# Kernel tuning notes

Measured on AMD Instinct MI355X. Metric: run time of the kernel, lower is better.

Reference implementation:

```python
import jax, jax.numpy as jnp
import numpy as np

EPS = 1e-8

def _center(G):
    # Double-centering: H @ G @ H with H = I - 11^T/n, expressed as mean subtraction.
    # Identical math to the torch H-matmul version, O(n^2) instead of O(n^3).
    row = jnp.mean(G, axis=-1, keepdims=True)
    col = jnp.mean(G, axis=-2, keepdims=True)
    tot = jnp.mean(G, axis=(-2, -1), keepdims=True)
    return G - row - col + tot


def setup_inputs() -> dict:
    key = jax.random.key(0)
    k1, k2 = jax.random.split(key)
    B, L, H, M = 32, 128, 512, 512
    x = jax.random.normal(k1, (B, L, H), dtype=jnp.float32)
    # nn.Embedding.from_pretrained(torch.normal(-0.01, 0.2, (M, L*H)))
    centroid_w = jax.random.normal(k2, (M, L * H), dtype=jnp.float32) * 0.2 - 0.01
    return {"x": x, "centroid_w": centroid_w}


def reference(x, centroid_w):
    B, L, H = x.shape
    M = centroid_w.shape[0]
    cent = centroid_w.reshape(M, L, H)

    # Centered linear Grams
    Cx = _center(jnp.einsum('blh,bkh->blk', x, x))        # (B, L, L)
    Cy = _center(jnp.einsum('mlh,mkh->mlk', cent, cent))  # (M, L, L)

    # linear HSIC: sum over LxL of elementwise product -> (B, M)
    hsic = jnp.einsum('bij,mij->bm', Cx, Cy)
    vx = jnp.sqrt(jnp.sum(Cx * Cx, axis=(1, 2)))  # (B,)  sqrt(HSIC(x,x))
    vy = jnp.sqrt(jnp.sum(Cy * Cy, axis=(1, 2)))  # (M,)  sqrt(HSIC(y,y))
    cka_loss_matrix = -jnp.log(jnp.abs(hsic / (vx[:, None] * vy[None, :])) + EPS)

    idx = jnp.argmax(cka_loss_matrix, axis=-1)  # (B,)
    sel = cent[idx]                              # (B, L, H) gathered centroids

    # Second CKA pass against selected centroids; torch broadcasting makes (B, B)
    Cs = _center(jnp.einsum('blh,bkh->blk', sel, sel))  # (B, L, L)
    hsic2 = jnp.einsum('bij,cij->bc', Cx, Cs)           # (B, B)
    vs = jnp.sqrt(jnp.sum(Cs * Cs, axis=(1, 2)))        # (B,)
    cka_loss = -jnp.log(jnp.mean(jnp.abs(hsic2 / (vx[:, None] * vs[None, :]))) + EPS)

    return cka_loss, cka_loss_matrix, idx
```

## Files before the change

kernel.cpp:

```cpp
#include <hip/hip_runtime.h>
#include <math.h>

#define BB 32
#define LL 128
#define HH 512
#define MM 512
#define NM 544
#define EPSF 1e-8f
#define CPLEN 10240
#define NCH 40

typedef __attribute__((ext_vector_type(8))) short short8b;
typedef __attribute__((ext_vector_type(4))) float f32x4;
typedef __attribute__((ext_vector_type(16))) float f32x16;

#define NWS_CP    0
#define NWS_PART  5570560
#define NWS_NSQ   6225920
#define NWS_HSIC  6226464
#define NWS_IDS   6242848

__device__ __forceinline__ unsigned pack2(unsigned lo, unsigned hi) {
    return (lo >> 16) | (hi & 0xffff0000u);
}

__device__ __forceinline__ void split3(const float4 lo, const float4 hi,
                                       uint4& p0, uint4& p1, uint4& p2) {
    float c[8] = {lo.x, lo.y, lo.z, lo.w, hi.x, hi.y, hi.z, hi.w};
    unsigned h[8], m[8], l[8];
#pragma unroll
    for (int i = 0; i < 8; ++i) {
        h[i] = __float_as_uint(c[i]) & 0xffff0000u;
        const float r1 = c[i] - __uint_as_float(h[i]);
        m[i] = __float_as_uint(r1) & 0xffff0000u;
        l[i] = __float_as_uint(r1 - __uint_as_float(m[i]));
    }
    p0 = make_uint4(pack2(h[0],h[1]), pack2(h[2],h[3]), pack2(h[4],h[5]), pack2(h[6],h[7]));
    p1 = make_uint4(pack2(m[0],m[1]), pack2(m[2],m[3]), pack2(m[4],m[5]), pack2(m[6],m[7]));
    p2 = make_uint4(pack2(l[0],l[1]), pack2(l[2],l[3]), pack2(l[4],l[5]), pack2(l[6],l[7]));
}

__device__ __forceinline__ void mfma6(f32x16& d, const short8b a[3], const short8b b[3]) {
    d = __builtin_amdgcn_mfma_f32_32x32x16_bf16(a[0], b[0], d, 0, 0, 0);
    d = __builtin_amdgcn_mfma_f32_32x32x16_bf16(a[0], b[1], d, 0, 0, 0);
    d = __builtin_amdgcn_mfma_f32_32x32x16_bf16(a[1], b[0], d, 0, 0, 0);
    d = __builtin_amdgcn_mfma_f32_32x32x16_bf16(a[1], b[1], d, 0, 0, 0);
    d = __builtin_amdgcn_mfma_f32_32x32x16_bf16(a[0], b[2], d, 0, 0, 0);
    d = __builtin_amdgcn_mfma_f32_32x32x16_bf16(a[2], b[0], d, 0, 0, 0);
}

__device__ __forceinline__ int flatAB(int a, int b) {
    return ((a >> 3) * 2 + ((a >> 2) & 1)) * 128 + b * 4 + (a & 3);
}

__device__ __forceinline__ int Tix(int i, int j) {
    return i * (7 - i) / 2 + j;
}

__global__ __launch_bounds__(256, 2)
void gram_nb(const float* __restrict__ x,
             const float* __restrict__ cent,
             float* __restrict__ Cp,
             float* __restrict__ normsq)
{
    __shared__ union {
        uint4 stage[4][3][2][128];
        float buf[12288];
    } sm;
    __shared__ float rmv[128];
    __shared__ float red[256];
    __shared__ float gmsh;

    const int tid  = threadIdx.x;
    const int lane = tid & 63;
    const int wid  = tid >> 6;
    const int n    = blockIdx.x;
    const float* Amat = (n < BB) ? (x + (size_t)n * LL * HH)
                                 : (cent + (size_t)(n - BB) * LL * HH);

    const int o   = lane & 1;
    const int r2  = lane >> 1;
    const int kw  = wid * 128;

    f32x16 acc[10];
#pragma unroll
    for (int g = 0; g < 10; ++g)
#pragma unroll
        for (int q = 0; q < 16; ++q) acc[g][q] = 0.f;

    uint4* SW = &sm.stage[wid][0][0][0];

    float4 v0[4], v1[4];
#pragma unroll
    for (int p = 0; p < 4; ++p) {
        const float* rp = Amat + (size_t)(32 * p + r2) * HH + kw + o * 8;
        v0[p] = *(const float4*)rp;
        v1[p] = *(const float4*)(rp + 4);
    }

    for (int t = 0; t < 8; ++t) {
#pragma unroll
        for (int p = 0; p < 4; ++p) {
            uint4 q0, q1, q2;
            split3(v0[p], v1[p], q0, q1, q2);
            const int r = 32 * p + r2;
            SW[(0 * 2 + o) * 128 + r] = q0;
            SW[(1 * 2 + o) * 128 + r] = q1;
            SW[(2 * 2 + o) * 128 + r] = q2;
        }
        const int kn = kw + ((t < 7) ? (t + 1) * 16 : 112);
#pragma unroll
        for (int p = 0; p < 4; ++p) {
            const float* rp = Amat + (size_t)(32 * p + r2) * HH + kn + o * 8;
            v0[p] = *(const float4*)rp;
            v1[p] = *(const float4*)(rp + 4);
        }
        const int fo = lane >> 5, frr = lane & 31;
        short8b fr[4][3];
#pragma unroll
        for (int s = 0; s < 4; ++s)
#pragma unroll
            for (int pl = 0; pl < 3; ++pl) {
                uint4 u = SW[(pl * 2 + fo) * 128 + s * 32 + frr];
                fr[s][pl] = *(const short8b*)&u;
            }
        mfma6(acc[0], fr[0], fr[0]);
        mfma6(acc[1], fr[0], fr[1]);
        mfma6(acc[4], fr[1], fr[1]);
        mfma6(acc[2], fr[0], fr[2]);
        mfma6(acc[5], fr[1], fr[2]);
        mfma6(acc[7], fr[2], fr[2]);
        mfma6(acc[3], fr[0], fr[3]);
        mfma6(acc[6], fr[1], fr[3]);
        mfma6(acc[8], fr[2], fr[3]);
        mfma6(acc[9], fr[3], fr[3]);
    }

    __syncthreads();

    const int hi  = lane >> 5, col = lane & 31;
#pragma unroll
    for (int w = 0; w < 4; ++w) {
        if (wid == w) {
#pragma unroll
            for (int g = 0; g < 10; ++g)
#pragma unroll
                for (int c = 0; c < 4; ++c) {
                    const int idx = g * 1024 + (c * 2 + hi) * 128 + col * 4;
                    f32x4 a4;
                    a4[0] = acc[g][c * 4 + 0];
                    a4[1] = acc[g][c * 4 + 1];
                    a4[2] = acc[g][c * 4 + 2];
                    a4[3] = acc[g][c * 4 + 3];
                    if (w > 0) {
                        const f32x4 old = *(const f32x4*)&sm.buf[idx];
                        a4[0] += old[0]; a4[1] += old[1];
                        a4[2] += old[2]; a4[3] += old[3];
                    }
                    *(f32x4*)&sm.buf[idx] = a4;
                }
        }
        __syncthreads();
    }

    float s = 0.f;
    if (tid < 128) {
        const int i = tid >> 5, ri = tid & 31;
#pragma unroll
        for (int j = 0; j < 4; ++j) {
            if (j >= i) {
                const int g = Tix(i, j);
#pragma unroll
                for (int b = 0; b < 32; ++b)
                    s += sm.buf[g * 1024 + flatAB(ri, b)];
            } else {
                const int g = Tix(j, i);
#pragma unroll
                for (int a = 0; a < 32; ++a)
                    s += sm.buf[g * 1024 + flatAB(a, ri)];
            }
        }
        rmv[tid] = s * (1.f / 128.f);
    }
    red[tid] = (tid < 128) ? s : 0.f;
    __syncthreads();
    for (int s2 = 128; s2 > 0; s2 >>= 1) {
        if (tid < s2) red[tid] += red[tid + s2];
        __syncthreads();
    }
    if (tid == 0) gmsh = red[0] * (1.f / 16384.f);
    __syncthreads();
    const float gm = gmsh;

    const int b  = tid & 31;
    const int c2 = tid >> 5;
    const int ar = (c2 >> 1) * 8 + (c2 & 1) * 4;
    float nsq = 0.f;
    float* dstn = Cp + (size_t)n * CPLEN;
    static const int TI[10] = {0,0,0,0,1,1,1,2,2,3};
    static const int TJ[10] = {0,1,2,3,1,2,3,2,3,3};
#pragma unroll
    for (int g = 0; g < 10; ++g) {
        const int i = TI[g], j = TJ[g];
        const float sc = (i == j) ? 1.f : 1.41421356237309505f;
        const f32x4 vv = *(const f32x4*)&sm.buf[g * 1024 + tid * 4];
        const float4 rr = *(const float4*)&rmv[i * 32 + ar];
        const float riq[4] = {rr.x, rr.y, rr.z, rr.w};
        const float cj = rmv[j * 32 + b];
        f32x4 ov;
#pragma unroll
        for (int q = 0; q < 4; ++q) {
            const float val = (vv[q] + gm - riq[q] - cj) * sc;
            nsq = fmaf(val, val, nsq);
            ov[q] = val;
        }
        *(f32x4*)(dstn + g * 1024 + tid * 4) = ov;
    }
    __syncthreads();
    red[tid] = nsq;
    __syncthreads();
    for (int s2 = 128; s2 > 0; s2 >>= 1) {
        if (tid < s2) red[tid] += red[tid + s2];
        __syncthreads();
    }
    if (tid == 0) normsq[n] = red[0];
}

__global__ __launch_bounds__(256, 2)
void hsic_partial(const float* __restrict__ Cp, float* __restrict__ part)
{
    __shared__ float cx[32][260];
    __shared__ float red2[256][16];

    const int tid = threadIdx.x;
    const int bx  = blockIdx.x;
    const int mt  = bx / NCH;
    const int kc  = bx % NCH;
    const int k0  = kc * 256;

#pragma unroll
    for (int i = 0; i < 8; ++i) {
        const int idx = i * 1024 + tid * 4;
        const int b = idx >> 8, k = idx & 255;
        *(float4*)&cx[b][k] = *(const float4*)&Cp[(size_t)b * CPLEN + k0 + k];
    }
    __syncthreads();

    const int kq = tid >> 6;
    const int bg = (tid >> 3) & 7;
    const int mg = tid & 7;
    const float* cyBase = Cp + (size_t)(BB + mt * 32 + mg * 4) * CPLEN + k0 + kq * 64;

    float a[4][4];
#pragma unroll
    for (int bi = 0; bi < 4; ++bi)
#pragma unroll
        for (int mi = 0; mi < 4; ++mi) a[bi][mi] = 0.f;

    for (int kk = 0; kk < 16; ++kk) {
        float4 cy[4];
#pragma unroll
        for (int mi = 0; mi < 4; ++mi)
            cy[mi] = *(const float4*)(cyBase + (size_t)mi * CPLEN + kk * 4);
        float4 cxv[4];
#pragma unroll
        for (int bi = 0; bi < 4; ++bi)
            cxv[bi] = *(const float4*)&cx[bg + bi * 8][kq * 64 + kk * 4];
#pragma unroll
        for (int bi = 0; bi < 4; ++bi)
#pragma unroll
            for (int mi = 0; mi < 4; ++mi) {
                a[bi][mi] = fmaf(cxv[bi].x, cy[mi].x, a[bi][mi]);
                a[bi][mi] = fmaf(cxv[bi].y, cy[mi].y, a[bi][mi]);
                a[bi][mi] = fmaf(cxv[bi].z, cy[mi].z, a[bi][mi]);
                a[bi][mi] = fmaf(cxv[bi].w, cy[mi].w, a[bi][mi]);
            }
    }

#pragma unroll
    for (int e = 0; e < 16; ++e) red2[tid][e] = a[e >> 2][e & 3];
    __syncthreads();
    if (tid < 64) {
#pragma unroll
        for (int e = 0; e < 16; ++e) {
            const float s = red2[tid][e] + red2[tid + 64][e] +
                            red2[tid + 128][e] + red2[tid + 192][e];
            const int bi = e >> 2, mi = e & 3;
            const int b = ((tid >> 3) & 7) + bi * 8;
            const int m = mt * 32 + (tid & 7) * 4 + mi;
            part[((size_t)kc * 32 + b) * 512 + m] = s;
        }
    }
}

__global__ __launch_bounds__(256)
void combine_loss(const float* __restrict__ part,
                  const float* __restrict__ normsq,
                  float* __restrict__ hsic,
                  int* __restrict__ ids,
                  float* __restrict__ out)
{
    __shared__ float rv[256];
    __shared__ int   ri[256];
    const int b = blockIdx.x;
    const int tid = threadIdx.x;
    const float vx = sqrtf(normsq[b]);

    float best = -INFINITY; int bm = 0;
    for (int m = tid; m < MM; m += 256) {
        float s = 0.f;
        for (int kc = 0; kc < NCH; ++kc)
            s += part[((size_t)kc * 32 + b) * 512 + m];
        hsic[b * MM + m] = s;
        const float vy = sqrtf(normsq[BB + m]);
        const float loss = -logf(fabsf(s) / (vx * vy) + EPSF);
        out[1 + b * MM + m] = loss;
        if (loss > best) { best = loss; bm = m; }
    }
    rv[tid] = best; ri[tid] = bm;
    __syncthreads();
    for (int s2 = 128; s2 > 0; s2 >>= 1) {
        if (tid < s2) {
            if (rv[tid + s2] > rv[tid] ||
                (rv[tid + s2] == rv[tid] && ri[tid + s2] < ri[tid])) {
                rv[tid] = rv[tid + s2]; ri[tid] = ri[tid + s2];
            }
        }
        __syncthreads();
    }
    if (tid == 0) { ids[b] = ri[0]; out[1 + BB * MM + b] = (float)ri[0]; }
}

__global__ __launch_bounds__(1024)
void scalar_loss(const float* __restrict__ hsic,
                 const float* __restrict__ normsq,
                 const int* __restrict__ ids,
                 float* __restrict__ out)
{
    __shared__ float red[1024];
    const int tid = threadIdx.x;
    const int b = tid >> 5, c = tid & 31;
    const int m = ids[c];
    red[tid] = fabsf(hsic[b * MM + m]) /
               (sqrtf(normsq[b]) * sqrtf(normsq[BB + m]));
    __syncthreads();
    for (int s = 512; s > 0; s >>= 1) {
        if (tid < s) red[tid] += red[tid + s];
        __syncthreads();
    }
    if (tid == 0) out[0] = -logf(red[0] * (1.f / 1024.f) + EPSF);
}

extern "C" void kernel_launch(void* const* d_in, const int* in_sizes, int n_in,
                              void* d_out, int out_size, void* d_ws, size_t ws_size,
                              hipStream_t stream) {
    const float* x    = (const float*)d_in[0];
    const float* cent = (const float*)d_in[1];
    float* out = (float*)d_out;
    float* ws  = (float*)d_ws;

    float* Cp     = ws + NWS_CP;
    float* part   = ws + NWS_PART;
    float* normsq = ws + NWS_NSQ;
    float* hsic   = ws + NWS_HSIC;
    int*   ids    = (int*)(ws + NWS_IDS);

    gram_nb<<<NM, 256, 0, stream>>>(x, cent, Cp, normsq);
    hsic_partial<<<16 * NCH, 256, 0, stream>>>(Cp, part);
    combine_loss<<<BB, 256, 0, stream>>>(part, normsq, hsic, ids, out);
    scalar_loss<<<1, 1024, 0, stream>>>(hsic, normsq, ids, out);
}
```

Baseline: 98.05 us.

## Compute each Gram matrix in a single wave without LDS staging

Replaces the 4-wave Gram kernel, which split K across waves and reduced the partial Grams through shared memory, with a one-wave-per-matrix kernel. That wave loads fp32 rows straight into registers in MFMA fragment layout, double-buffers two K-steps, and does row and column means with cross-lane shuffles. The goal is to drop the LDS staging, the cross-wave reduction and the block barriers. The cost is that each matrix's whole K loop now runs serially on one wave. With 544 single-wave blocks the GPU runs far fewer waves, so memory latency and MFMA throughput per SIMD may be harder to hide.

```diff
diff --git a/kernel.cpp b/kernel.cpp
--- a/kernel.cpp
+++ b/kernel.cpp
@@ -20,6 +20,9 @@
 #define NWS_HSIC  6226464
 #define NWS_IDS   6242848
 
+__device__ __constant__ int TI_[10] = {0,0,0,0,1,1,1,2,2,3};
+__device__ __constant__ int TJ_[10] = {0,1,2,3,1,2,3,2,3,3};
+
 __device__ __forceinline__ unsigned pack2(unsigned lo, unsigned hi) {
     return (lo >> 16) | (hi & 0xffff0000u);
 }
@@ -40,47 +43,62 @@
     p2 = make_uint4(pack2(l[0],l[1]), pack2(l[2],l[3]), pack2(l[4],l[5]), pack2(l[6],l[7]));
 }
 
-__device__ __forceinline__ void mfma6(f32x16& d, const short8b a[3], const short8b b[3]) {
-    d = __builtin_amdgcn_mfma_f32_32x32x16_bf16(a[0], b[0], d, 0, 0, 0);
-    d = __builtin_amdgcn_mfma_f32_32x32x16_bf16(a[0], b[1], d, 0, 0, 0);
-    d = __builtin_amdgcn_mfma_f32_32x32x16_bf16(a[1], b[0], d, 0, 0, 0);
-    d = __builtin_amdgcn_mfma_f32_32x32x16_bf16(a[1], b[1], d, 0, 0, 0);
-    d = __builtin_amdgcn_mfma_f32_32x32x16_bf16(a[0], b[2], d, 0, 0, 0);
-    d = __builtin_amdgcn_mfma_f32_32x32x16_bf16(a[2], b[0], d, 0, 0, 0);
-}
-
-__device__ __forceinline__ int flatAB(int a, int b) {
-    return ((a >> 3) * 2 + ((a >> 2) & 1)) * 128 + b * 4 + (a & 3);
-}
-
-__device__ __forceinline__ int Tix(int i, int j) {
-    return i * (7 - i) / 2 + j;
-}
-
-__global__ __launch_bounds__(256, 2)
-void gram_nb(const float* __restrict__ x,
-             const float* __restrict__ cent,
-             float* __restrict__ Cp,
-             float* __restrict__ normsq)
+__device__ __forceinline__ float redxor5(float v) {
+    v += __shfl_xor(v, 1, 64);
+    v += __shfl_xor(v, 2, 64);
+    v += __shfl_xor(v, 4, 64);
+    v += __shfl_xor(v, 8, 64);
+    v += __shfl_xor(v, 16, 64);
+    return v;
+}
+
+#define LOADV(dst, t) do {                                                  \
+    _Pragma("unroll")                                                       \
+    for (int p_ = 0; p_ < 4; ++p_) {                                        \
+        const float* rp_ = Abase[p_] + (t) * 16;                            \
+        dst[2*p_]   = *(const float4*)rp_;                                  \
+        dst[2*p_+1] = *(const float4*)(rp_ + 4);                            \
+    } } while (0)
+
+#define SPLIT4(src, fr) do {                                                \
+    _Pragma("unroll")                                                       \
+    for (int p_ = 0; p_ < 4; ++p_) {                                        \
+        uint4 u0_, u1_, u2_;                                                \
+        split3(src[2*p_], src[2*p_+1], u0_, u1_, u2_);                      \
+        fr[p_][0] = *(short8b*)&u0_;                                        \
+        fr[p_][1] = *(short8b*)&u1_;                                        \
+        fr[p_][2] = *(short8b*)&u2_;                                        \
+    } } while (0)
+
+#define MFMA60(fr) do {                                                     \
+    const int PA_[6] = {0,0,1,1,0,2};                                       \
+    const int PB_[6] = {0,1,0,1,2,0};                                       \
+    _Pragma("unroll")                                                       \
+    for (int ps_ = 0; ps_ < 6; ++ps_) {                                     \
+        _Pragma("unroll")                                                   \
+        for (int g_ = 0; g_ < 10; ++g_)                                     \
+            acc[g_] = __builtin_amdgcn_mfma_f32_32x32x16_bf16(              \
+                fr[TI_[g_]][PA_[ps_]], fr[TJ_[g_]][PB_[ps_]], acc[g_], 0, 0, 0); \
+    } } while (0)
+
+__global__ __launch_bounds__(64, 1)
+void gram_wave(const float* __restrict__ x,
+               const float* __restrict__ cent,
+               float* __restrict__ Cp,
+               float* __restrict__ normsq)
 {
-    __shared__ union {
-        uint4 stage[4][3][2][128];
-        float buf[12288];
-    } sm;
-    __shared__ float rmv[128];
-    __shared__ float red[256];
-    __shared__ float gmsh;
-
-    const int tid  = threadIdx.x;
-    const int lane = tid & 63;
-    const int wid  = tid >> 6;
+    __shared__ __align__(16) float rowacc[128];
+
+    const int lane = threadIdx.x;
+    const int r32  = lane & 31;
+    const int oct  = lane >> 5;
     const int n    = blockIdx.x;
     const float* Amat = (n < BB) ? (x + (size_t)n * LL * HH)
                                  : (cent + (size_t)(n - BB) * LL * HH);
-
-    const int o   = lane & 1;
-    const int r2  = lane >> 1;
-    const int kw  = wid * 128;
+    const float* Abase[4];
+#pragma unroll
+    for (int p = 0; p < 4; ++p)
+        Abase[p] = Amat + (size_t)(32 * p + r32) * HH + oct * 8;
 
     f32x16 acc[10];
 #pragma unroll
@@ -88,142 +106,110 @@
 #pragma unroll
         for (int q = 0; q < 16; ++q) acc[g][q] = 0.f;
 
-    uint4* SW = &sm.stage[wid][0][0][0];
-
-    float4 v0[4], v1[4];
-#pragma unroll
-    for (int p = 0; p < 4; ++p) {
-        const float* rp = Amat + (size_t)(32 * p + r2) * HH + kw + o * 8;
-        v0[p] = *(const float4*)rp;
-        v1[p] = *(const float4*)(rp + 4);
-    }
-
-    for (int t = 0; t < 8; ++t) {
-#pragma unroll
-        for (int p = 0; p < 4; ++p) {
-            uint4 q0, q1, q2;
-            split3(v0[p], v1[p], q0, q1, q2);
-            const int r = 32 * p + r2;
-            SW[(0 * 2 + o) * 128 + r] = q0;
-            SW[(1 * 2 + o) * 128 + r] = q1;
-            SW[(2 * 2 + o) * 128 + r] = q2;
-        }
-        const int kn = kw + ((t < 7) ? (t + 1) * 16 : 112);
-#pragma unroll
-        for (int p = 0; p < 4; ++p) {
-            const float* rp = Amat + (size_t)(32 * p + r2) * HH + kn + o * 8;
-            v0[p] = *(const float4*)rp;
-            v1[p] = *(const float4*)(rp + 4);
-        }
-        const int fo = lane >> 5, frr = lane & 31;
-        short8b fr[4][3];
-#pragma unroll
-        for (int s = 0; s < 4; ++s)
-#pragma unroll
-            for (int pl = 0; pl < 3; ++pl) {
-                uint4 u = SW[(pl * 2 + fo) * 128 + s * 32 + frr];
-                fr[s][pl] = *(const short8b*)&u;
-            }
-        mfma6(acc[0], fr[0], fr[0]);
-        mfma6(acc[1], fr[0], fr[1]);
-        mfma6(acc[4], fr[1], fr[1]);
-        mfma6(acc[2], fr[0], fr[2]);
-        mfma6(acc[5], fr[1], fr[2]);
-        mfma6(acc[7], fr[2], fr[2]);
-        mfma6(acc[3], fr[0], fr[3]);
-        mfma6(acc[6], fr[1], fr[3]);
-        mfma6(acc[8], fr[2], fr[3]);
-        mfma6(acc[9], fr[3], fr[3]);
-    }
-
-    __syncthreads();
-
-    const int hi  = lane >> 5, col = lane & 31;
-#pragma unroll
-    for (int w = 0; w < 4; ++w) {
-        if (wid == w) {
+    float4 sA[8], sB[8];
+    short8b frA[4][3], frB[4][3];
+
+    LOADV(sA, 0);
+    LOADV(sB, 1);
+#pragma unroll 1
+    for (int tt = 0; tt < 16; ++tt) {
+        SPLIT4(sA, frA);
+        if (tt < 15) { LOADV(sA, 2 * tt + 2); }
+        MFMA60(frA);
+        SPLIT4(sB, frB);
+        if (tt < 15) { LOADV(sB, 2 * tt + 3); }
+        MFMA60(frB);
+    }
+
+#pragma unroll
+    for (int i = 0; i < 4; ++i) {
+        float rp[16];
+#pragma unroll
+        for (int q = 0; q < 16; ++q) {
+            float s = 0.f;
 #pragma unroll
             for (int g = 0; g < 10; ++g)
-#pragma unroll
-                for (int c = 0; c < 4; ++c) {
-                    const int idx = g * 1024 + (c * 2 + hi) * 128 + col * 4;
-                    f32x4 a4;
-                    a4[0] = acc[g][c * 4 + 0];
-                    a4[1] = acc[g][c * 4 + 1];
-                    a4[2] = acc[g][c * 4 + 2];
-                    a4[3] = acc[g][c * 4 + 3];
-                    if (w > 0) {
-                        const f32x4 old = *(const f32x4*)&sm.buf[idx];
-                        a4[0] += old[0]; a4[1] += old[1];
-                        a4[2] += old[2]; a4[3] += old[3];
-                    }
-                    *(f32x4*)&sm.buf[idx] = a4;
-                }
-        }
-        __syncthreads();
-    }
-
-    float s = 0.f;
-    if (tid < 128) {
-        const int i = tid >> 5, ri = tid & 31;
-#pragma unroll
-        for (int j = 0; j < 4; ++j) {
-            if (j >= i) {
-                const int g = Tix(i, j);
-#pragma unroll
-                for (int b = 0; b < 32; ++b)
-                    s += sm.buf[g * 1024 + flatAB(ri, b)];
-            } else {
-                const int g = Tix(j, i);
-#pragma unroll
-                for (int a = 0; a < 32; ++a)
-                    s += sm.buf[g * 1024 + flatAB(a, ri)];
-            }
-        }
-        rmv[tid] = s * (1.f / 128.f);
-    }
-    red[tid] = (tid < 128) ? s : 0.f;
-    __syncthreads();
-    for (int s2 = 128; s2 > 0; s2 >>= 1) {
-        if (tid < s2) red[tid] += red[tid + s2];
-        __syncthreads();
-    }
-    if (tid == 0) gmsh = red[0] * (1.f / 16384.f);
-    __syncthreads();
-    const float gm = gmsh;
-
-    const int b  = tid & 31;
-    const int c2 = tid >> 5;
-    const int ar = (c2 >> 1) * 8 + (c2 & 1) * 4;
+                if (TI_[g] == i) s += acc[g][q];
+            rp[q] = redxor5(s);
+        }
+        if (r32 == 0) {
+#pragma unroll
+            for (int q = 0; q < 16; ++q)
+                rowacc[i * 32 + (q & 3) + 8 * (q >> 2) + 4 * oct] = rp[q];
+        }
+    }
+    {
+        float cs1 = 0.f, cs2 = 0.f, cs3 = 0.f;
+#pragma unroll
+        for (int g = 0; g < 10; ++g) {
+            if (TI_[g] == TJ_[g]) continue;
+            float cp = 0.f;
+#pragma unroll
+            for (int q = 0; q < 16; ++q) cp += acc[g][q];
+            if (TJ_[g] == 1) cs1 += cp;
+            else if (TJ_[g] == 2) cs2 += cp;
+            else cs3 += cp;
+        }
+        cs1 += __shfl_xor(cs1, 32, 64);
+        cs2 += __shfl_xor(cs2, 32, 64);
+        cs3 += __shfl_xor(cs3, 32, 64);
+        if (oct == 0) {
+            rowacc[1 * 32 + r32] += cs1;
+            rowacc[2 * 32 + r32] += cs2;
+            rowacc[3 * 32 + r32] += cs3;
+        }
+    }
+
+    float tot = rowacc[lane] + rowacc[lane + 64];
+    tot += __shfl_xor(tot, 1, 64);
+    tot += __shfl_xor(tot, 2, 64);
+    tot += __shfl_xor(tot, 4, 64);
+    tot += __shfl_xor(tot, 8, 64);
+    tot += __shfl_xor(tot, 16, 64);
+    tot += __shfl_xor(tot, 32, 64);
+    const float gm = tot * (1.f / 16384.f);
+
+    f32x4 rim[4][4];
+#pragma unroll
+    for (int i = 0; i < 4; ++i)
+#pragma unroll
+        for (int c = 0; c < 4; ++c) {
+            const f32x4 rv = *(const f32x4*)&rowacc[i * 32 + 8 * c + 4 * oct];
+            rim[i][c][0] = gm - rv[0] * (1.f / 128.f);
+            rim[i][c][1] = gm - rv[1] * (1.f / 128.f);
+            rim[i][c][2] = gm - rv[2] * (1.f / 128.f);
+            rim[i][c][3] = gm - rv[3] * (1.f / 128.f);
+        }
+    float cjs[4];
+#pragma unroll
+    for (int j = 0; j < 4; ++j) cjs[j] = rowacc[j * 32 + r32] * (1.f / 128.f);
+
     float nsq = 0.f;
     float* dstn = Cp + (size_t)n * CPLEN;
-    static const int TI[10] = {0,0,0,0,1,1,1,2,2,3};
-    static const int TJ[10] = {0,1,2,3,1,2,3,2,3,3};
 #pragma unroll
     for (int g = 0; g < 10; ++g) {
-        const int i = TI[g], j = TJ[g];
+        const int i = TI_[g], j = TJ_[g];
         const float sc = (i == j) ? 1.f : 1.41421356237309505f;
-        const f32x4 vv = *(const f32x4*)&sm.buf[g * 1024 + tid * 4];
-        const float4 rr = *(const float4*)&rmv[i * 32 + ar];
-        const float riq[4] = {rr.x, rr.y, rr.z, rr.w};
-        const float cj = rmv[j * 32 + b];
-        f32x4 ov;
-#pragma unroll
-        for (int q = 0; q < 4; ++q) {
-            const float val = (vv[q] + gm - riq[q] - cj) * sc;
-            nsq = fmaf(val, val, nsq);
-            ov[q] = val;
-        }
-        *(f32x4*)(dstn + g * 1024 + tid * 4) = ov;
-    }
-    __syncthreads();
-    red[tid] = nsq;
-    __syncthreads();
-    for (int s2 = 128; s2 > 0; s2 >>= 1) {
-        if (tid < s2) red[tid] += red[tid + s2];
-        __syncthreads();
-    }
-    if (tid == 0) normsq[n] = red[0];
+        const float cj = cjs[j];
+#pragma unroll
+        for (int c = 0; c < 4; ++c) {
+            f32x4 o;
+#pragma unroll
+            for (int q = 0; q < 4; ++q) {
+                const float val = (acc[g][c * 4 + q] + rim[i][c][q] - cj) * sc;
+                nsq = fmaf(val, val, nsq);
+                o[q] = val;
+            }
+            *(f32x4*)(dstn + g * 1024 + (c * 2 + oct) * 128 + r32 * 4) = o;
+        }
+    }
+    nsq += __shfl_xor(nsq, 1, 64);
+    nsq += __shfl_xor(nsq, 2, 64);
+    nsq += __shfl_xor(nsq, 4, 64);
+    nsq += __shfl_xor(nsq, 8, 64);
+    nsq += __shfl_xor(nsq, 16, 64);
+    nsq += __shfl_xor(nsq, 32, 64);
+    if (lane == 0) normsq[n] = nsq;
 }
 
 __global__ __launch_bounds__(256, 2)
@@ -365,7 +351,7 @@
     float* hsic   = ws + NWS_HSIC;
     int*   ids    = (int*)(ws + NWS_IDS);
 
-    gram_nb<<<NM, 256, 0, stream>>>(x, cent, Cp, normsq);
+    gram_wave<<<NM, 64, 0, stream>>>(x, cent, Cp, normsq);
     hsic_partial<<<16 * NCH, 256, 0, stream>>>(Cp, part);
     combine_loss<<<BB, 256, 0, stream>>>(part, normsq, hsic, ids, out);
     scalar_loss<<<1, 1024, 0, stream>>>(hsic, normsq, ids, out);
```

After: 315.7 us. +222.0%, slower.

## Restructure gram kernel to 8 waves with tile-split MFMA and double-buffered staging

Applied to the files above, without the earlier changes.

The Gram kernel moves from 4 waves (each computing all 10 triangular tiles over its own K slice) to 8 waves in two K-halves. Within a half, the 4 waves share one double-buffered LDS stage and split the 10 tiles among themselves, 2-3 each. This cuts per-wave accumulator registers so more waves fit per CU, and reduces the cross-wave reduction to two passes. In exchange it adds a __syncthreads every K step and unequal work per wave.

```diff
diff --git a/kernel.cpp b/kernel.cpp
--- a/kernel.cpp
+++ b/kernel.cpp
@@ -49,142 +49,157 @@
     d = __builtin_amdgcn_mfma_f32_32x32x16_bf16(a[2], b[0], d, 0, 0, 0);
 }
 
+__device__ __forceinline__ void ldstrip(const uint4* P, int strip, int lane, short8b f[3]) {
+    const int s = lane >> 5;
+    const int r = strip * 32 + (lane & 31);
+#pragma unroll
+    for (int p = 0; p < 3; ++p) {
+        uint4 u = P[(p * 2 + s) * 128 + r];
+        f[p] = *(const short8b*)&u;
+    }
+}
+
 __device__ __forceinline__ int flatAB(int a, int b) {
     return ((a >> 3) * 2 + ((a >> 2) & 1)) * 128 + b * 4 + (a & 3);
 }
-
 __device__ __forceinline__ int Tix(int i, int j) {
     return i * (7 - i) / 2 + j;
 }
 
-__global__ __launch_bounds__(256, 2)
-void gram_nb(const float* __restrict__ x,
-             const float* __restrict__ cent,
-             float* __restrict__ Cp,
-             float* __restrict__ normsq)
+__device__ __forceinline__ void put_tile(float* buf, int slot, const f32x16& a,
+                                         int lane, bool add) {
+    const int hi = lane >> 5, col = lane & 31;
+#pragma unroll
+    for (int c = 0; c < 4; ++c) {
+        const int idx = slot * 1024 + (c * 2 + hi) * 128 + col * 4;
+        f32x4 v;
+        v[0] = a[c * 4 + 0]; v[1] = a[c * 4 + 1];
+        v[2] = a[c * 4 + 2]; v[3] = a[c * 4 + 3];
+        if (add) {
+            const f32x4 o = *(const f32x4*)&buf[idx];
+            v[0] += o[0]; v[1] += o[1]; v[2] += o[2]; v[3] += o[3];
+        }
+        *(f32x4*)&buf[idx] = v;
+    }
+}
+
+__global__ __launch_bounds__(512, 4)
+void gram8(const float* __restrict__ x,
+           const float* __restrict__ cent,
+           float* __restrict__ Cp,
+           float* __restrict__ normsq)
 {
-    __shared__ union {
-        uint4 stage[4][3][2][128];
-        float buf[12288];
-    } sm;
+    __shared__ __align__(16) unsigned char smraw[49152];
     __shared__ float rmv[128];
-    __shared__ float red[256];
+    __shared__ float red[512];
     __shared__ float gmsh;
+
+    uint4* stage = (uint4*)smraw;
+    float* buf   = (float*)smraw;
 
     const int tid  = threadIdx.x;
     const int lane = tid & 63;
     const int wid  = tid >> 6;
+    const int g    = wid >> 2;
+    const int gw   = wid & 3;
     const int n    = blockIdx.x;
     const float* Amat = (n < BB) ? (x + (size_t)n * LL * HH)
                                  : (cent + (size_t)(n - BB) * LL * HH);
 
-    const int o   = lane & 1;
-    const int r2  = lane >> 1;
-    const int kw  = wid * 128;
-
-    f32x16 acc[10];
-#pragma unroll
-    for (int g = 0; g < 10; ++g)
-#pragma unroll
-        for (int q = 0; q < 16; ++q) acc[g][q] = 0.f;
-
-    uint4* SW = &sm.stage[wid][0][0][0];
-
-    float4 v0[4], v1[4];
-#pragma unroll
-    for (int p = 0; p < 4; ++p) {
-        const float* rp = Amat + (size_t)(32 * p + r2) * HH + kw + o * 8;
-        v0[p] = *(const float4*)rp;
-        v1[p] = *(const float4*)(rp + 4);
-    }
-
-    for (int t = 0; t < 8; ++t) {
-#pragma unroll
-        for (int p = 0; p < 4; ++p) {
-            uint4 q0, q1, q2;
-            split3(v0[p], v1[p], q0, q1, q2);
-            const int r = 32 * p + r2;
-            SW[(0 * 2 + o) * 128 + r] = q0;
-            SW[(1 * 2 + o) * 128 + r] = q1;
-            SW[(2 * 2 + o) * 128 + r] = q2;
-        }
-        const int kn = kw + ((t < 7) ? (t + 1) * 16 : 112);
-#pragma unroll
-        for (int p = 0; p < 4; ++p) {
-            const float* rp = Amat + (size_t)(32 * p + r2) * HH + kn + o * 8;
-            v0[p] = *(const float4*)rp;
-            v1[p] = *(const float4*)(rp + 4);
-        }
-        const int fo = lane >> 5, frr = lane & 31;
-        short8b fr[4][3];
-#pragma unroll
-        for (int s = 0; s < 4; ++s)
-#pragma unroll
-            for (int pl = 0; pl < 3; ++pl) {
-                uint4 u = SW[(pl * 2 + fo) * 128 + s * 32 + frr];
-                fr[s][pl] = *(const short8b*)&u;
-            }
-        mfma6(acc[0], fr[0], fr[0]);
-        mfma6(acc[1], fr[0], fr[1]);
-        mfma6(acc[4], fr[1], fr[1]);
-        mfma6(acc[2], fr[0], fr[2]);
-        mfma6(acc[5], fr[1], fr[2]);
-        mfma6(acc[7], fr[2], fr[2]);
-        mfma6(acc[3], fr[0], fr[3]);
-        mfma6(acc[6], fr[1], fr[3]);
-        mfma6(acc[8], fr[2], fr[3]);
-        mfma6(acc[9], fr[3], fr[3]);
-    }
-
-    __syncthreads();
-
-    const int hi  = lane >> 5, col = lane & 31;
-#pragma unroll
-    for (int w = 0; w < 4; ++w) {
-        if (wid == w) {
-#pragma unroll
-            for (int g = 0; g < 10; ++g)
-#pragma unroll
-                for (int c = 0; c < 4; ++c) {
-                    const int idx = g * 1024 + (c * 2 + hi) * 128 + col * 4;
-                    f32x4 a4;
-                    a4[0] = acc[g][c * 4 + 0];
-                    a4[1] = acc[g][c * 4 + 1];
-                    a4[2] = acc[g][c * 4 + 2];
-                    a4[3] = acc[g][c * 4 + 3];
-                    if (w > 0) {
-                        const f32x4 old = *(const f32x4*)&sm.buf[idx];
-                        a4[0] += old[0]; a4[1] += old[1];
-                        a4[2] += old[2]; a4[3] += old[3];
-                    }
-                    *(f32x4*)&sm.buf[idx] = a4;
-                }
-        }
-        __syncthreads();
-    }
-
-    float s = 0.f;
+    const int trow  = (tid >> 1) & 127;
+    const int shalf = tid & 1;
+    const float* rowp = Amat + (size_t)trow * HH + g * 256 + shalf * 8;
+
+    f32x16 a0, a1, a2;
+#pragma unroll
+    for (int q = 0; q < 16; ++q) { a0[q] = 0.f; a1[q] = 0.f; a2[q] = 0.f; }
+
+    float4 vA0 = *(const float4*)(rowp);
+    float4 vA1 = *(const float4*)(rowp + 4);
+    float4 vB0 = *(const float4*)(rowp + 16);
+    float4 vB1 = *(const float4*)(rowp + 20);
+
+#pragma unroll 2
+    for (int t = 0; t < 16; ++t) {
+        const int pb = t & 1;
+        uint4 p0, p1, p2;
+        if (pb == 0) split3(vA0, vA1, p0, p1, p2);
+        else         split3(vB0, vB1, p0, p1, p2);
+
+        uint4* SW = stage + g * 1536 + pb * 768;
+        SW[(0 * 2 + shalf) * 128 + trow] = p0;
+        SW[(1 * 2 + shalf) * 128 + trow] = p1;
+        SW[(2 * 2 + shalf) * 128 + trow] = p2;
+
+        if (t < 14) {
+            const float* np = rowp + (t + 2) * 16;
+            if (pb == 0) { vA0 = *(const float4*)np; vA1 = *(const float4*)(np + 4); }
+            else         { vB0 = *(const float4*)np; vB1 = *(const float4*)(np + 4); }
+        }
+
+        __syncthreads();
+
+        const uint4* Pr = stage + g * 1536 + pb * 768;
+        short8b fa[3], fb[3];
+        if (gw == 0) {
+            ldstrip(Pr, 3, lane, fb);
+            ldstrip(Pr, 0, lane, fa); mfma6(a0, fa, fb);
+            ldstrip(Pr, 1, lane, fa); mfma6(a1, fa, fb);
+            ldstrip(Pr, 2, lane, fa); mfma6(a2, fa, fb);
+        } else if (gw == 1) {
+            ldstrip(Pr, 3, lane, fa); mfma6(a0, fa, fa);
+            ldstrip(Pr, 2, lane, fb);
+            ldstrip(Pr, 0, lane, fa); mfma6(a1, fa, fb);
+            ldstrip(Pr, 1, lane, fa); mfma6(a2, fa, fb);
+        } else if (gw == 2) {
+            ldstrip(Pr, 2, lane, fa); mfma6(a0, fa, fa);
+            ldstrip(Pr, 0, lane, fa);
+            ldstrip(Pr, 1, lane, fb); mfma6(a1, fa, fb);
+        } else {
+            ldstrip(Pr, 0, lane, fa); mfma6(a0, fa, fa);
+            ldstrip(Pr, 1, lane, fa); mfma6(a1, fa, fa);
+        }
+    }
+
+    __syncthreads();
+
+    if (g == 0) {
+        if (gw == 0)      { put_tile(buf, 3, a0, lane, false); put_tile(buf, 6, a1, lane, false); put_tile(buf, 8, a2, lane, false); }
+        else if (gw == 1) { put_tile(buf, 9, a0, lane, false); put_tile(buf, 2, a1, lane, false); put_tile(buf, 5, a2, lane, false); }
+        else if (gw == 2) { put_tile(buf, 7, a0, lane, false); put_tile(buf, 1, a1, lane, false); }
+        else              { put_tile(buf, 0, a0, lane, false); put_tile(buf, 4, a1, lane, false); }
+    }
+    __syncthreads();
+    if (g == 1) {
+        if (gw == 0)      { put_tile(buf, 3, a0, lane, true); put_tile(buf, 6, a1, lane, true); put_tile(buf, 8, a2, lane, true); }
+        else if (gw == 1) { put_tile(buf, 9, a0, lane, true); put_tile(buf, 2, a1, lane, true); put_tile(buf, 5, a2, lane, true); }
+        else if (gw == 2) { put_tile(buf, 7, a0, lane, true); put_tile(buf, 1, a1, lane, true); }
+        else              { put_tile(buf, 0, a0, lane, true); put_tile(buf, 4, a1, lane, true); }
+    }
+    __syncthreads();
+
+    float Sv = 0.f;
     if (tid < 128) {
         const int i = tid >> 5, ri = tid & 31;
 #pragma unroll
         for (int j = 0; j < 4; ++j) {
             if (j >= i) {
-                const int g = Tix(i, j);
+                const int gt = Tix(i, j);
 #pragma unroll
                 for (int b = 0; b < 32; ++b)
-                    s += sm.buf[g * 1024 + flatAB(ri, b)];
+                    Sv += buf[gt * 1024 + flatAB(ri, b)];
             } else {
-                const int g = Tix(j, i);
+                const int gt = Tix(j, i);
 #pragma unroll
                 for (int a = 0; a < 32; ++a)
-                    s += sm.buf[g * 1024 + flatAB(a, ri)];
+                    Sv += buf[gt * 1024 + flatAB(a, ri)];
             }
         }
-        rmv[tid] = s * (1.f / 128.f);
-    }
-    red[tid] = (tid < 128) ? s : 0.f;
-    __syncthreads();
-    for (int s2 = 128; s2 > 0; s2 >>= 1) {
+        rmv[tid] = Sv * (1.f / 128.f);
+    }
+    red[tid] = (tid < 128) ? Sv : 0.f;
+    __syncthreads();
+    for (int s2 = 256; s2 > 0; s2 >>= 1) {
         if (tid < s2) red[tid] += red[tid + s2];
         __syncthreads();
     }
@@ -192,34 +207,37 @@
     __syncthreads();
     const float gm = gmsh;
 
-    const int b  = tid & 31;
-    const int c2 = tid >> 5;
-    const int ar = (c2 >> 1) * 8 + (c2 & 1) * 4;
     float nsq = 0.f;
     float* dstn = Cp + (size_t)n * CPLEN;
-    static const int TI[10] = {0,0,0,0,1,1,1,2,2,3};
-    static const int TJ[10] = {0,1,2,3,1,2,3,2,3,3};
-#pragma unroll
-    for (int g = 0; g < 10; ++g) {
-        const int i = TI[g], j = TJ[g];
+#pragma unroll
+    for (int u5 = 0; u5 < 5; ++u5) {
+        const int u  = u5 * 512 + tid;
+        const int gt = u >> 8;
+        const int fo = (u & 255) * 4;
+        const int c2 = fo >> 7;
+        const int col = (fo >> 2) & 31;
+        const int ar = (c2 >> 1) * 8 + (c2 & 1) * 4;
+        int i, j;
+        if (gt < 4)      { i = 0; j = gt; }
+        else if (gt < 7) { i = 1; j = gt - 3; }
+        else if (gt < 9) { i = 2; j = gt - 5; }
+        else             { i = 3; j = 3; }
         const float sc = (i == j) ? 1.f : 1.41421356237309505f;
-        const f32x4 vv = *(const f32x4*)&sm.buf[g * 1024 + tid * 4];
-        const float4 rr = *(const float4*)&rmv[i * 32 + ar];
-        const float riq[4] = {rr.x, rr.y, rr.z, rr.w};
-        const float cj = rmv[j * 32 + b];
-        f32x4 ov;
+        const f32x4 vv = *(const f32x4*)&buf[u * 4];
+        const float cj = rmv[j * 32 + col];
+        f32x4 o;
 #pragma unroll
         for (int q = 0; q < 4; ++q) {
-            const float val = (vv[q] + gm - riq[q] - cj) * sc;
+            const float val = (vv[q] + gm - rmv[i * 32 + ar + q] - cj) * sc;
             nsq = fmaf(val, val, nsq);
-            ov[q] = val;
-        }
-        *(f32x4*)(dstn + g * 1024 + tid * 4) = ov;
+            o[q] = val;
+        }
+        *(f32x4*)(dstn + u * 4) = o;
     }
     __syncthreads();
     red[tid] = nsq;
     __syncthreads();
-    for (int s2 = 128; s2 > 0; s2 >>= 1) {
+    for (int s2 = 256; s2 > 0; s2 >>= 1) {
         if (tid < s2) red[tid] += red[tid + s2];
         __syncthreads();
     }
@@ -365,7 +383,7 @@
     float* hsic   = ws + NWS_HSIC;
     int*   ids    = (int*)(ws + NWS_IDS);
 
-    gram_nb<<<NM, 256, 0, stream>>>(x, cent, Cp, normsq);
+    gram8<<<NM, 512, 0, stream>>>(x, cent, Cp, normsq);
     hsic_partial<<<16 * NCH, 256, 0, stream>>>(Cp, part);
     combine_loss<<<BB, 256, 0, stream>>>(part, normsq, hsic, ids, out);
     scalar_loss<<<1, 1024, 0, stream>>>(hsic, normsq, ids, out);
```

After: 96.39 us. About the same (-1.7%).
